# Performance work log

Hardware: AMD Instinct MI355X
Metric: run time of the kernel (lower is better)

The kernel has to match this reference:

```python
import jax, jax.numpy as jnp
import numpy as np

B, S, D, H = 2, 2048, 1024, 16
DK = D // H


def layernorm(x, gamma, bias, eps=1e-6):
    m = jnp.mean(x, axis=-1, keepdims=True)
    v = jnp.mean((x - m) ** 2, axis=-1, keepdims=True)  # biased var (correction=0)
    return gamma * (x - m) / jnp.sqrt(v + eps) + bias


def setup_inputs() -> dict:
    key = jax.random.key(0)
    ks = jax.random.split(key, 10)
    xav = (2.0 / (D + D)) ** 0.5  # xavier_normal_ std for square [D,D]
    lin1_b = (1.0 / D) ** 0.5     # nn.Linear default init bound
    lin2_b = (1.0 / (4 * D)) ** 0.5
    return {
        "X": jax.random.normal(ks[0], (B, S, D), jnp.float32),
        "padding_mask": jnp.ones((B, 1, S), jnp.int32),
        "W_Q": jax.random.normal(ks[1], (D, D), jnp.float32) * xav,
        "W_K": jax.random.normal(ks[2], (D, D), jnp.float32) * xav,
        "W_V": jax.random.normal(ks[3], (D, D), jnp.float32) * xav,
        "W_O": jax.random.normal(ks[4], (D, D), jnp.float32) * xav,
        "g1": jnp.ones((D,), jnp.float32),
        "b1": jnp.zeros((D,), jnp.float32),
        "W1": jax.random.uniform(ks[5], (D, 4 * D), jnp.float32, -lin1_b, lin1_b),
        "bias1": jax.random.uniform(ks[6], (4 * D,), jnp.float32, -lin1_b, lin1_b),
        "W2": jax.random.uniform(ks[7], (4 * D, D), jnp.float32, -lin2_b, lin2_b),
        "bias2": jax.random.uniform(ks[8], (D,), jnp.float32, -lin2_b, lin2_b),
        "g2": jnp.ones((D,), jnp.float32),
        "b2": jnp.zeros((D,), jnp.float32),
    }


def reference(X, padding_mask, W_Q, W_K, W_V, W_O, g1, b1, W1, bias1, W2, bias2, g2, b2):
    b, s, d = X.shape
    # pre-norm + MHA
    xn = layernorm(X, g1, b1)
    q = (xn @ W_Q).reshape(b, s, H, DK).transpose(0, 2, 1, 3)  # [B,H,S,DK]
    k = (xn @ W_K).reshape(b, s, H, DK).transpose(0, 2, 1, 3)
    v = (xn @ W_V).reshape(b, s, H, DK).transpose(0, 2, 1, 3)
    scores = jnp.einsum("bhqd,bhkd->bhqk", q, k) / np.sqrt(DK).astype(np.float32)
    mask = padding_mask[:, None, :, :]  # [B,1,1,S] broadcast over heads/queries
    scores = jnp.where(mask == 0, jnp.float32(-1e9), scores)
    w = jax.nn.softmax(scores, axis=-1)
    attn = jnp.einsum("bhqk,bhkd->bhqd", w, v)
    attn = attn.transpose(0, 2, 1, 3).reshape(b, s, d) @ W_O
    out = attn + X
    # pre-norm + GELU FFN (exact erf GELU, matching nn.GELU default)
    nn2 = layernorm(out, g2, b2)
    ff = jax.nn.gelu(nn2 @ W1 + bias1, approximate=False) @ W2 + bias2
    return ff + out
```

## Files before the change

### kernel.cpp

```cpp
#include <hip/hip_runtime.h>
#include <hip/hip_bf16.h>


using bf16 = __hip_bfloat16;
typedef __attribute__((ext_vector_type(4))) float f32x4;
typedef __attribute__((ext_vector_type(16))) float f32x16;
typedef __attribute__((ext_vector_type(8))) short bf16x8;

#define DEVI static __device__ __forceinline__

DEVI void async_copy16(const void* g, void* l) {
  __builtin_amdgcn_global_load_lds(
      (const __attribute__((address_space(1))) void*)g,
      (__attribute__((address_space(3))) void*)l, 16, 0, 0);
}

DEVI ushort f2bf_bits(float v) {
  __hip_bfloat16 h = __float2bfloat16(v);
  return *reinterpret_cast<ushort*>(&h);
}

DEVI float bfbits2f(ushort u) {
  union { float f; unsigned int i; } x;
  x.i = ((unsigned int)u) << 16;
  return x.f;
}

DEVI unsigned int pk2(float lo, float hi) {
  return (unsigned int)f2bf_bits(lo) | ((unsigned int)f2bf_bits(hi) << 16);
}

__global__ __launch_bounds__(256) void ln_kernel(
    const float* __restrict__ in, const float* __restrict__ gamma,
    const float* __restrict__ beta, bf16* __restrict__ out) {
  const long row = blockIdx.x;
  const int t = threadIdx.x;
  float4 x = ((const float4*)(in + row * 1024))[t];
  float s = x.x + x.y + x.z + x.w;
  float s2 = x.x * x.x + x.y * x.y + x.z * x.z + x.w * x.w;
#pragma unroll
  for (int m = 1; m < 64; m <<= 1) {
    s += __shfl_xor(s, m);
    s2 += __shfl_xor(s2, m);
  }
  __shared__ float red[8];
  const int w = t >> 6, l = t & 63;
  if (l == 0) { red[w] = s; red[4 + w] = s2; }
  __syncthreads();
  s = red[0] + red[1] + red[2] + red[3];
  s2 = red[4] + red[5] + red[6] + red[7];
  const float mean = s * (1.0f / 1024.0f);
  const float var = s2 * (1.0f / 1024.0f) - mean * mean;
  const float rstd = rsqrtf(var + 1e-6f);
  float4 g4 = ((const float4*)gamma)[t];
  float4 b4 = ((const float4*)beta)[t];
  union { ushort h[4]; uint2 u; } o;
  o.h[0] = f2bf_bits(g4.x * (x.x - mean) * rstd + b4.x);
  o.h[1] = f2bf_bits(g4.y * (x.y - mean) * rstd + b4.y);
  o.h[2] = f2bf_bits(g4.z * (x.z - mean) * rstd + b4.z);
  o.h[3] = f2bf_bits(g4.w * (x.w - mean) * rstd + b4.w);
  ((uint2*)(out + row * 1024))[t] = o.u;
}

__global__ __launch_bounds__(256) void transpose_to_bf16(
    const float* __restrict__ W, bf16* __restrict__ Wt, const int K, const int N) {
  __shared__ float tile[32][33];
  const int tx = threadIdx.x & 31, ty = threadIdx.x >> 5;
  const int n0 = blockIdx.x << 5, k0 = blockIdx.y << 5;
#pragma unroll
  for (int i = 0; i < 32; i += 8)
    tile[ty + i][tx] = W[(long)(k0 + ty + i) * N + n0 + tx];
  __syncthreads();
#pragma unroll
  for (int i = 0; i < 32; i += 8)
    Wt[(long)(n0 + ty + i) * K + k0 + tx] = __float2bfloat16(tile[tx][ty + i]);
}

__global__ __launch_bounds__(256) void transpose_qkvo(
    const float* __restrict__ q, const float* __restrict__ k,
    const float* __restrict__ v, const float* __restrict__ o,
    bf16* __restrict__ dst) {
  const float* W = (blockIdx.z == 0) ? q : (blockIdx.z == 1) ? k
                   : (blockIdx.z == 2) ? v : o;
  bf16* Wt = dst + (size_t)blockIdx.z * 1024 * 1024;
  __shared__ float tile[32][33];
  const int tx = threadIdx.x & 31, ty = threadIdx.x >> 5;
  const int n0 = blockIdx.x << 5, k0 = blockIdx.y << 5;
#pragma unroll
  for (int i = 0; i < 32; i += 8)
    tile[ty + i][tx] = W[(long)(k0 + ty + i) * 1024 + n0 + tx];
  __syncthreads();
#pragma unroll
  for (int i = 0; i < 32; i += 8)
    Wt[(long)(n0 + ty + i) * 1024 + k0 + tx] = __float2bfloat16(tile[tx][ty + i]);
}

template <int EPI, int KSPLIT>
__global__ __launch_bounds__(256) void gemm_bt(
    const bf16* __restrict__ A, const bf16* __restrict__ Bt,
    const int M, const int N, const int K, const int lda, const int ldb,
    const float* __restrict__ bias, const float* __restrict__ res,
    float* __restrict__ pother, void* __restrict__ Cout) {
  __shared__ bf16 As[128 * 32];
  __shared__ bf16 Bs[128 * 32];
  const int t = threadIdx.x;
  const int w = t >> 6, l = t & 63;
  const int nb = N >> 7;
  const int cpx = gridDim.x >> 3;
  int bidx = (blockIdx.x & 7) * cpx + (blockIdx.x >> 3);
  int sl = 0;
  if (KSPLIT == 2) {
    const int half = gridDim.x >> 1;
    sl = bidx >= half;
    bidx -= sl * half;
  }
  const int bm = bidx / nb, bn = bidx % nb;
  const long row0 = (long)bm << 7, col0 = (long)bn << 7;
  const int wr = (w >> 1) << 6, wc = (w & 1) << 6;
  const int lr = l & 15, lk = (l >> 4) << 3;

  f32x4 acc[4][4];
#pragma unroll
  for (int m = 0; m < 4; ++m)
#pragma unroll
    for (int n = 0; n < 4; ++n) acc[m][n] = (f32x4){0.f, 0.f, 0.f, 0.f};

  const bf16* gA = A + (row0 + (t >> 2)) * (long)lda + (long)sl * K + ((t & 3) << 3);
  const bf16* gB = Bt + (col0 + (t >> 2)) * (long)ldb + (long)sl * K + ((t & 3) << 3);
  char* lA = (char*)As + (w << 10);
  char* lB = (char*)Bs + (w << 10);
  const long k64a = (long)64 * lda, k64b = (long)64 * ldb;

  for (int k0 = 0; k0 < K; k0 += 32) {
    __syncthreads();
    async_copy16(gA + k0, lA);
    async_copy16(gA + k64a + k0, lA + 4096);
    async_copy16(gB + k0, lB);
    async_copy16(gB + k64b + k0, lB + 4096);
    __syncthreads();
    bf16x8 af[4], bfr[4];
#pragma unroll
    for (int m = 0; m < 4; ++m)
      af[m] = *(const bf16x8*)&As[(wr + m * 16 + lr) * 32 + lk];
#pragma unroll
    for (int n = 0; n < 4; ++n)
      bfr[n] = *(const bf16x8*)&Bs[(wc + n * 16 + lr) * 32 + lk];
#pragma unroll
    for (int m = 0; m < 4; ++m)
#pragma unroll
      for (int n = 0; n < 4; ++n)
        acc[m][n] = __builtin_amdgcn_mfma_f32_16x16x32_bf16(af[m], bfr[n], acc[m][n], 0, 0, 0);
  }

  bf16* Cb = (bf16*)Cout;
  float* Cf = (float*)Cout;
  if (EPI == 4 && sl == 1) Cf = pother;
#pragma unroll
  for (int m = 0; m < 4; ++m) {
#pragma unroll
    for (int r = 0; r < 4; ++r) {
      const long crow = row0 + wr + m * 16 + ((l >> 4) << 2) + r;
      const long rbase = crow * N;
#pragma unroll
      for (int n = 0; n < 4; ++n) {
        const long ccol = col0 + wc + n * 16 + lr;
        float v = acc[m][n][r];
        if (EPI == 2) {
          v += bias[ccol];
          v = 0.5f * v * (1.0f + erff(v * 0.70710678118654752f));
        }
        if (EPI == 1) v += res[rbase + ccol];
        if (EPI == 0 || EPI == 2)
          Cb[rbase + ccol] = __float2bfloat16(v);
        else
          Cf[rbase + ccol] = v;
      }
    }
  }
}

__global__ __launch_bounds__(256) void ff2_reduce(
    const float* __restrict__ p0, const float* __restrict__ p1,
    const float* __restrict__ bias, float* __restrict__ out) {
  const int idx = blockIdx.x * 256 + threadIdx.x;
  float4 a = ((const float4*)out)[idx];
  const float4 x = ((const float4*)p0)[idx];
  const float4 y = ((const float4*)p1)[idx];
  const float4 bb = ((const float4*)bias)[idx & 255];
  a.x += x.x + y.x + bb.x;
  a.y += x.y + y.y + bb.y;
  a.z += x.z + y.z + bb.z;
  a.w += x.w + y.w + bb.w;
  ((float4*)out)[idx] = a;
}

__global__ __launch_bounds__(256) void attn_kernel(
    const bf16* __restrict__ QKV, const int* __restrict__ pmask,
    bf16* __restrict__ Oout) {
  const int bh = blockIdx.y;
  const int b = bh >> 4, h = bh & 15;
  const int q0 = blockIdx.x << 7;
  const int t = threadIdx.x;
  const int w = t >> 6, l = t & 63;
  const int lq = l & 31, hi = l >> 5;

  __shared__ __align__(16) char smem[32768];

  const long base = (long)b * 2048 * 3072;
  const bf16* Qg = QKV + base + h * 64;
  const bf16* Kg = QKV + base + 1024 + h * 64;
  const bf16* Vg = QKV + base + 2048 + h * 64;

  int kSrc[2];
#pragma unroll
  for (int p = 0; p < 2; ++p) {
    const int r = w * 16 + p * 8 + (l >> 3);
    kSrc[p] = r * 3072 + (((l & 7) ^ (r & 7)) << 3);
  }
  const int vr0 = t >> 3, vsg = t & 7;

  const int qw0 = q0 + w * 32;
  bf16x8 qf[4];
#pragma unroll
  for (int dc = 0; dc < 4; ++dc) {
    uint4 raw = *(const uint4*)(Qg + (long)(qw0 + lq) * 3072 + dc * 16 + hi * 8);
    union { uint4 u4; ushort us[8]; } in; in.u4 = raw;
    union { bf16x8 v; ushort us[8]; } o;
#pragma unroll
    for (int e = 0; e < 8; ++e) o.us[e] = f2bf_bits(0.18033688011f * bfbits2f(in.us[e]));
    qf[dc] = o.v;
  }

  union { unsigned int u[4]; bf16x8 v; } bones;
  bones.u[0] = (hi == 0) ? 0x00003F80u : 0u;
  bones.u[1] = bones.u[2] = bones.u[3] = 0u;

  uint4 vreg[2];
#pragma unroll
  for (int p = 0; p < 2; ++p) {
    vreg[p] = *(const uint4*)(Vg + (long)(p * 32 + vr0) * 3072 + vsg * 8);
    async_copy16(Kg + kSrc[p], smem + w * 2048 + p * 1024);
  }
#pragma unroll
  for (int p = 0; p < 2; ++p) {
    const int r = p * 32 + vr0;
    const ushort* vs = (const ushort*)&vreg[p];
#pragma unroll
    for (int e = 0; e < 8; ++e) {
      const int d = vsg * 8 + e;
      *(ushort*)(smem + 16384 + d * 128 + ((r * 2) ^ (((e ^ vsg) & 7) << 4))) = vs[e];
    }
  }

  f32x16 oacc[2];
#pragma unroll
  for (int nt = 0; nt < 2; ++nt)
#pragma unroll
    for (int r = 0; r < 16; ++r) oacc[nt][r] = 0.f;
  float mrun = -3.0e38f, lsum = 0.f;
  int cur = 0;

  __syncthreads();

  for (int ktg = 0; ktg < 32; ++ktg) {
    if (ktg < 31) {
      const long nrow0 = (long)(ktg + 1) * 64 * 3072;
#pragma unroll
      for (int p = 0; p < 2; ++p) {
        vreg[p] = *(const uint4*)(Vg + nrow0 + (long)(p * 32 + vr0) * 3072 + vsg * 8);
        async_copy16(Kg + nrow0 + kSrc[p], smem + (cur ^ 1) * 8192 + w * 2048 + p * 1024);
      }
    }
    const int k0 = ktg << 6;
    const char* Ks = smem + cur * 8192;
    const char* Vt = smem + 16384 + cur * 8192;

    f32x16 sacc[2];
#pragma unroll
    for (int kt = 0; kt < 2; ++kt) {
#pragma unroll
      for (int r = 0; r < 16; ++r) sacc[kt][r] = 0.f;
#pragma unroll
      for (int dc = 0; dc < 4; ++dc) {
        bf16x8 ka = *(const bf16x8*)(Ks +
            ((kt * 32 + lq) * 128 + ((dc * 32 + hi * 16) ^ ((lq & 7) << 4))));
        sacc[kt] = __builtin_amdgcn_mfma_f32_32x32x16_bf16(ka, qf[dc], sacc[kt], 0, 0, 0);
      }
      const int mv = pmask[b * 2048 + k0 + kt * 32 + lq];
      union { unsigned int u[4]; bf16x8 v; } aadd;
      aadd.u[0] = (hi == 0 && mv == 0) ? (unsigned int)f2bf_bits(-1.0e9f) : 0u;
      aadd.u[1] = aadd.u[2] = aadd.u[3] = 0u;
      sacc[kt] = __builtin_amdgcn_mfma_f32_32x32x16_bf16(aadd.v, bones.v, sacc[kt], 0, 0, 0);
    }

    float tmax = -3.0e38f;
#pragma unroll
    for (int kt = 0; kt < 2; ++kt)
#pragma unroll
      for (int r = 0; r < 16; ++r) tmax = fmaxf(tmax, sacc[kt][r]);
    tmax = fmaxf(tmax, __shfl_xor(tmax, 32));
    const bool need = (bool)__any(tmax > mrun + 8.0f);
    const float mnew = need ? fmaxf(mrun, tmax) : mrun;
    float psum = 0.f;
#pragma unroll
    for (int kt = 0; kt < 2; ++kt)
#pragma unroll
      for (int r = 0; r < 16; ++r) {
        const float p = exp2f(sacc[kt][r] - mnew);
        sacc[kt][r] = p;
        psum += p;
      }
    psum += __shfl_xor(psum, 32);
    if (need) {
      const float alpha = exp2f(mrun - mnew);
      mrun = mnew;
      lsum = lsum * alpha + psum;
#pragma unroll
      for (int r = 0; r < 16; ++r) {
        const float ar = __shfl(alpha, (r & 3) + 8 * (r >> 2) + 4 * hi);
        oacc[0][r] *= ar;
        oacc[1][r] *= ar;
      }
    } else {
      lsum += psum;
    }

    union { unsigned int u[4]; bf16x8 v; } paE[2], paO[2];
#pragma unroll
    for (int kt = 0; kt < 2; ++kt) {
      const unsigned int cs0 = pk2(sacc[kt][0], sacc[kt][1]);
      const unsigned int cs1 = pk2(sacc[kt][2], sacc[kt][3]);
      const unsigned int cs2 = pk2(sacc[kt][4], sacc[kt][5]);
      const unsigned int cs3 = pk2(sacc[kt][6], sacc[kt][7]);
      const unsigned int cs4 = pk2(sacc[kt][8], sacc[kt][9]);
      const unsigned int cs5 = pk2(sacc[kt][10], sacc[kt][11]);
      const unsigned int cs6 = pk2(sacc[kt][12], sacc[kt][13]);
      const unsigned int cs7 = pk2(sacc[kt][14], sacc[kt][15]);
      const unsigned int es0 = __shfl_xor(cs0, 32);
      const unsigned int es1 = __shfl_xor(cs1, 32);
      const unsigned int es2 = __shfl_xor(cs2, 32);
      const unsigned int es3 = __shfl_xor(cs3, 32);
      const unsigned int es4 = __shfl_xor(cs4, 32);
      const unsigned int es5 = __shfl_xor(cs5, 32);
      const unsigned int es6 = __shfl_xor(cs6, 32);
      const unsigned int es7 = __shfl_xor(cs7, 32);
      paE[kt].u[0] = hi ? es2 : cs0;
      paE[kt].u[1] = hi ? es3 : cs1;
      paE[kt].u[2] = hi ? cs2 : es0;
      paE[kt].u[3] = hi ? cs3 : es1;
      paO[kt].u[0] = hi ? es6 : cs4;
      paO[kt].u[1] = hi ? es7 : cs5;
      paO[kt].u[2] = hi ? cs6 : es4;
      paO[kt].u[3] = hi ? cs7 : es5;
    }

#pragma unroll
    for (int kt = 0; kt < 2; ++kt)
#pragma unroll
      for (int nt = 0; nt < 2; ++nt) {
        const int vrow = nt * 32 + lq;
        const int vsw = ((vrow & 7) ^ ((vrow >> 3) & 7)) << 4;
        bf16x8 vbE = *(const bf16x8*)(Vt + (vrow * 128 + ((kt * 64 + hi * 16) ^ vsw)));
        oacc[nt] = __builtin_amdgcn_mfma_f32_32x32x16_bf16(paE[kt].v, vbE, oacc[nt], 0, 0, 0);
        bf16x8 vbO = *(const bf16x8*)(Vt + (vrow * 128 + ((kt * 64 + 32 + hi * 16) ^ vsw)));
        oacc[nt] = __builtin_amdgcn_mfma_f32_32x32x16_bf16(paO[kt].v, vbO, oacc[nt], 0, 0, 0);
      }

    if (ktg < 31) {
      char* VtN = smem + 16384 + (cur ^ 1) * 8192;
#pragma unroll
      for (int p = 0; p < 2; ++p) {
        const int r = p * 32 + vr0;
        const ushort* vs = (const ushort*)&vreg[p];
#pragma unroll
        for (int e = 0; e < 8; ++e) {
          const int d = vsg * 8 + e;
          *(ushort*)(VtN + d * 128 + ((r * 2) ^ (((e ^ vsg) & 7) << 4))) = vs[e];
        }
      }
    }

    __syncthreads();
    cur ^= 1;
  }

  const float inv = 1.0f / lsum;
#pragma unroll
  for (int r = 0; r < 16; ++r) {
    const int crow = (r & 3) + 8 * (r >> 2) + 4 * hi;
    const float ir = __shfl(inv, crow);
    const long orow = (long)b * 2048 + qw0 + crow;
#pragma unroll
    for (int nt = 0; nt < 2; ++nt)
      Oout[orow * 1024 + h * 64 + nt * 32 + lq] = __float2bfloat16(oacc[nt][r] * ir);
  }
}

extern "C" void kernel_launch(void* const* d_in, const int* in_sizes, int n_in,
                              void* d_out, int out_size, void* d_ws, size_t ws_size,
                              hipStream_t stream) {
  const float* X = (const float*)d_in[0];
  const int* pmask = (const int*)d_in[1];
  const float* W_Q = (const float*)d_in[2];
  const float* W_K = (const float*)d_in[3];
  const float* W_V = (const float*)d_in[4];
  const float* W_O = (const float*)d_in[5];
  const float* g1 = (const float*)d_in[6];
  const float* b1 = (const float*)d_in[7];
  const float* W1 = (const float*)d_in[8];
  const float* bias1 = (const float*)d_in[9];
  const float* W2 = (const float*)d_in[10];
  const float* bias2 = (const float*)d_in[11];
  const float* g2 = (const float*)d_in[12];
  const float* b2 = (const float*)d_in[13];
  (void)in_sizes; (void)n_in; (void)out_size; (void)ws_size;

  char* ws = (char*)d_ws;
  const size_t MB = 1ull << 20;
  bf16* W1_t   = (bf16*)(ws + 0);
  bf16* Wqkv_t = (bf16*)(ws + 8 * MB);
  bf16* Wo_t   = (bf16*)(ws + 14 * MB);
  bf16* W2_t   = (bf16*)(ws + 16 * MB);
  bf16* xn     = (bf16*)(ws + 24 * MB);
  bf16* QKV    = (bf16*)(ws + 32 * MB);
  bf16* attnb  = (bf16*)(ws + 56 * MB);
  bf16* ff1    = (bf16*)(ws + 32 * MB);
  float* p0    = (float*)(ws + 64 * MB);
  float* p1    = (float*)(ws + 0);
  float* res1  = (float*)d_out;

  transpose_qkvo<<<dim3(32, 32, 4), 256, 0, stream>>>(W_Q, W_K, W_V, W_O, Wqkv_t);
  transpose_to_bf16<<<dim3(128, 32), 256, 0, stream>>>(W1, W1_t, 1024, 4096);
  transpose_to_bf16<<<dim3(32, 128), 256, 0, stream>>>(W2, W2_t, 4096, 1024);

  ln_kernel<<<4096, 256, 0, stream>>>(X, g1, b1, xn);
  gemm_bt<0, 1><<<32 * 24, 256, 0, stream>>>(xn, Wqkv_t, 4096, 3072, 1024, 1024, 1024,
                                             nullptr, nullptr, nullptr, QKV);
  attn_kernel<<<dim3(16, 32), 256, 0, stream>>>(QKV, pmask, attnb);
  gemm_bt<1, 1><<<32 * 8, 256, 0, stream>>>(attnb, Wo_t, 4096, 1024, 1024, 1024, 1024,
                                            nullptr, X, nullptr, res1);
  ln_kernel<<<4096, 256, 0, stream>>>(res1, g2, b2, xn);
  gemm_bt<2, 1><<<32 * 32, 256, 0, stream>>>(xn, W1_t, 4096, 4096, 1024, 1024, 1024,
                                             bias1, nullptr, nullptr, ff1);
  gemm_bt<4, 2><<<2 * 32 * 8, 256, 0, stream>>>(ff1, W2_t, 4096, 1024, 2048, 4096, 4096,
                                                nullptr, nullptr, p1, p0);
  ff2_reduce<<<4096, 256, 0, stream>>>(p0, p1, bias2, res1);
}
```

Measured before the change: 322.7 us.

## Widen attention blocks to 512 threads and fuse FF2 bias/residual into GEMM epilogue

Attention now launches 8-wave blocks covering 256 query rows each, with each wave loading one K/V chunk per tile, and the grid dimensions are swapped. The softmax switches from exp2 with a prescaled log2e to __expf and drops the lazy-rescale threshold, so rescaling happens on every max increase. The FF2 bias and residual adds move into the split-K GEMM epilogue, letting the reduce kernel read two buffers instead of four. The goals are better occupancy and less memory traffic in the reduce step, at the cost of more frequent rescaling work.

Measured after the change: 323.8 us. Within noise of the previous version (+0.3%).

```diff
diff --git a/kernel.cpp b/kernel.cpp
--- a/kernel.cpp
+++ b/kernel.cpp
@@ -154,7 +154,7 @@
 
   bf16* Cb = (bf16*)Cout;
   float* Cf = (float*)Cout;
-  if (EPI == 4 && sl == 1) Cf = pother;
+  if ((EPI == 4 || EPI == 5) && sl == 1) Cf = pother;
 #pragma unroll
   for (int m = 0; m < 4; ++m) {
 #pragma unroll
@@ -170,6 +170,7 @@
           v = 0.5f * v * (1.0f + erff(v * 0.70710678118654752f));
         }
         if (EPI == 1) v += res[rbase + ccol];
+        if (EPI == 5 && sl == 0) v += bias[ccol] + res[rbase + ccol];
         if (EPI == 0 || EPI == 2)
           Cb[rbase + ccol] = __float2bfloat16(v);
         else
@@ -181,25 +182,21 @@
 
 __global__ __launch_bounds__(256) void ff2_reduce(
     const float* __restrict__ p0, const float* __restrict__ p1,
-    const float* __restrict__ bias, float* __restrict__ out) {
+    float* __restrict__ out) {
   const int idx = blockIdx.x * 256 + threadIdx.x;
-  float4 a = ((const float4*)out)[idx];
   const float4 x = ((const float4*)p0)[idx];
   const float4 y = ((const float4*)p1)[idx];
-  const float4 bb = ((const float4*)bias)[idx & 255];
-  a.x += x.x + y.x + bb.x;
-  a.y += x.y + y.y + bb.y;
-  a.z += x.z + y.z + bb.z;
-  a.w += x.w + y.w + bb.w;
+  float4 a;
+  a.x = x.x + y.x; a.y = x.y + y.y; a.z = x.z + y.z; a.w = x.w + y.w;
   ((float4*)out)[idx] = a;
 }
 
-__global__ __launch_bounds__(256) void attn_kernel(
+__global__ __launch_bounds__(512) void attn_kernel(
     const bf16* __restrict__ QKV, const int* __restrict__ pmask,
     bf16* __restrict__ Oout) {
-  const int bh = blockIdx.y;
+  const int bh = blockIdx.x;
   const int b = bh >> 4, h = bh & 15;
-  const int q0 = blockIdx.x << 7;
+  const int q0 = blockIdx.y << 8;
   const int t = threadIdx.x;
   const int w = t >> 6, l = t & 63;
   const int lq = l & 31, hi = l >> 5;
@@ -211,12 +208,8 @@
   const bf16* Kg = QKV + base + 1024 + h * 64;
   const bf16* Vg = QKV + base + 2048 + h * 64;
 
-  int kSrc[2];
-#pragma unroll
-  for (int p = 0; p < 2; ++p) {
-    const int r = w * 16 + p * 8 + (l >> 3);
-    kSrc[p] = r * 3072 + (((l & 7) ^ (r & 7)) << 3);
-  }
+  const int kr = w * 8 + (l >> 3);
+  const int kSrc = kr * 3072 + (((l & 7) ^ (kr & 7)) << 3);
   const int vr0 = t >> 3, vsg = t & 7;
 
   const int qw0 = q0 + w * 32;
@@ -227,7 +220,7 @@
     union { uint4 u4; ushort us[8]; } in; in.u4 = raw;
     union { bf16x8 v; ushort us[8]; } o;
 #pragma unroll
-    for (int e = 0; e < 8; ++e) o.us[e] = f2bf_bits(0.18033688011f * bfbits2f(in.us[e]));
+    for (int e = 0; e < 8; ++e) o.us[e] = f2bf_bits(0.125f * bfbits2f(in.us[e]));
     qf[dc] = o.v;
   }
 
@@ -235,20 +228,14 @@
   bones.u[0] = (hi == 0) ? 0x00003F80u : 0u;
   bones.u[1] = bones.u[2] = bones.u[3] = 0u;
 
-  uint4 vreg[2];
-#pragma unroll
-  for (int p = 0; p < 2; ++p) {
-    vreg[p] = *(const uint4*)(Vg + (long)(p * 32 + vr0) * 3072 + vsg * 8);
-    async_copy16(Kg + kSrc[p], smem + w * 2048 + p * 1024);
-  }
-#pragma unroll
-  for (int p = 0; p < 2; ++p) {
-    const int r = p * 32 + vr0;
-    const ushort* vs = (const ushort*)&vreg[p];
+  uint4 vreg = *(const uint4*)(Vg + (long)vr0 * 3072 + vsg * 8);
+  async_copy16(Kg + kSrc, smem + w * 1024);
+  {
+    const ushort* vs = (const ushort*)&vreg;
 #pragma unroll
     for (int e = 0; e < 8; ++e) {
       const int d = vsg * 8 + e;
-      *(ushort*)(smem + 16384 + d * 128 + ((r * 2) ^ (((e ^ vsg) & 7) << 4))) = vs[e];
+      *(ushort*)(smem + 16384 + d * 128 + ((vr0 * 2) ^ (((e ^ vsg) & 7) << 4))) = vs[e];
     }
   }
 
@@ -265,11 +252,8 @@
   for (int ktg = 0; ktg < 32; ++ktg) {
     if (ktg < 31) {
       const long nrow0 = (long)(ktg + 1) * 64 * 3072;
-#pragma unroll
-      for (int p = 0; p < 2; ++p) {
-        vreg[p] = *(const uint4*)(Vg + nrow0 + (long)(p * 32 + vr0) * 3072 + vsg * 8);
-        async_copy16(Kg + nrow0 + kSrc[p], smem + (cur ^ 1) * 8192 + w * 2048 + p * 1024);
-      }
+      vreg = *(const uint4*)(Vg + nrow0 + (long)vr0 * 3072 + vsg * 8);
+      async_copy16(Kg + nrow0 + kSrc, smem + (cur ^ 1) * 8192 + w * 1024);
     }
     const int k0 = ktg << 6;
     const char* Ks = smem + cur * 8192;
@@ -299,20 +283,20 @@
 #pragma unroll
       for (int r = 0; r < 16; ++r) tmax = fmaxf(tmax, sacc[kt][r]);
     tmax = fmaxf(tmax, __shfl_xor(tmax, 32));
-    const bool need = (bool)__any(tmax > mrun + 8.0f);
+    const bool need = (bool)__any(tmax > mrun);
     const float mnew = need ? fmaxf(mrun, tmax) : mrun;
     float psum = 0.f;
 #pragma unroll
     for (int kt = 0; kt < 2; ++kt)
 #pragma unroll
       for (int r = 0; r < 16; ++r) {
-        const float p = exp2f(sacc[kt][r] - mnew);
+        const float p = __expf(sacc[kt][r] - mnew);
         sacc[kt][r] = p;
         psum += p;
       }
     psum += __shfl_xor(psum, 32);
     if (need) {
-      const float alpha = exp2f(mrun - mnew);
+      const float alpha = __expf(mrun - mnew);
       mrun = mnew;
       lsum = lsum * alpha + psum;
 #pragma unroll
@@ -368,15 +352,11 @@
 
     if (ktg < 31) {
       char* VtN = smem + 16384 + (cur ^ 1) * 8192;
-#pragma unroll
-      for (int p = 0; p < 2; ++p) {
-        const int r = p * 32 + vr0;
-        const ushort* vs = (const ushort*)&vreg[p];
-#pragma unroll
-        for (int e = 0; e < 8; ++e) {
-          const int d = vsg * 8 + e;
-          *(ushort*)(VtN + d * 128 + ((r * 2) ^ (((e ^ vsg) & 7) << 4))) = vs[e];
-        }
+      const ushort* vs = (const ushort*)&vreg;
+#pragma unroll
+      for (int e = 0; e < 8; ++e) {
+        const int d = vsg * 8 + e;
+        *(ushort*)(VtN + d * 128 + ((vr0 * 2) ^ (((e ^ vsg) & 7) << 4))) = vs[e];
       }
     }
 
@@ -436,13 +416,13 @@
   ln_kernel<<<4096, 256, 0, stream>>>(X, g1, b1, xn);
   gemm_bt<0, 1><<<32 * 24, 256, 0, stream>>>(xn, Wqkv_t, 4096, 3072, 1024, 1024, 1024,
                                              nullptr, nullptr, nullptr, QKV);
-  attn_kernel<<<dim3(16, 32), 256, 0, stream>>>(QKV, pmask, attnb);
+  attn_kernel<<<dim3(32, 8), 512, 0, stream>>>(QKV, pmask, attnb);
   gemm_bt<1, 1><<<32 * 8, 256, 0, stream>>>(attnb, Wo_t, 4096, 1024, 1024, 1024, 1024,
                                             nullptr, X, nullptr, res1);
   ln_kernel<<<4096, 256, 0, stream>>>(res1, g2, b2, xn);
   gemm_bt<2, 1><<<32 * 32, 256, 0, stream>>>(xn, W1_t, 4096, 4096, 1024, 1024, 1024,
                                              bias1, nullptr, nullptr, ff1);
-  gemm_bt<4, 2><<<2 * 32 * 8, 256, 0, stream>>>(ff1, W2_t, 4096, 1024, 2048, 4096, 4096,
-                                                nullptr, nullptr, p1, p0);
-  ff2_reduce<<<4096, 256, 0, stream>>>(p0, p1, bias2, res1);
-}
+  gemm_bt<5, 2><<<2 * 32 * 8, 256, 0, stream>>>(ff1, W2_t, 4096, 1024, 2048, 4096, 4096,
+                                                bias2, res1, p1, p0);
+  ff2_reduce<<<4096, 256, 0, stream>>>(p0, p1, res1);
+}
```
